# Kernel optimization log

Hardware: AMD Instinct MI355X
Metric: run time of the kernel (lower is better)

Reference implementation:

```python
import jax, jax.numpy as jnp
import numpy as np

B, L, D = 16384, 32, 128
DIAG_LEN, PROC_LEN, MED_LEN = 100000, 50000, 1000


def setup_inputs() -> dict:
    key = jax.random.key(0)
    ks = jax.random.split(key, 12)
    inp = {
        "diag_codes": jax.random.randint(ks[0], (B, L), 0, DIAG_LEN),
        "proc_codes": jax.random.randint(ks[1], (B, L), 0, PROC_LEN),
        "prev_diag_codes": jax.random.randint(ks[2], (B, L), 0, DIAG_LEN),
        "prev_proc_codes": jax.random.randint(ks[3], (B, L), 0, PROC_LEN),
        # learned parameters (torch Linear convention: W[out,in], y = x @ W.T + b)
        "diag_emb": jax.random.normal(ks[4], (DIAG_LEN, D), jnp.float32) * 0.02,
        "proc_emb": jax.random.normal(ks[5], (PROC_LEN, D), jnp.float32) * 0.02,
        "W1": jax.random.normal(ks[6], (D, 2 * D), jnp.float32) * 0.02,
        "b1": jnp.zeros((D,), jnp.float32),
        "W2": jax.random.normal(ks[7], (256, 2 * D), jnp.float32) * 0.02,
        "b2": jnp.zeros((256,), jnp.float32),
        "W3": jax.random.normal(ks[8], (MED_LEN, 256), jnp.float32) * 0.02,
        "b3": jnp.zeros((MED_LEN,), jnp.float32),
    }
    return inp


def _bag_sum(table, idx):
    # EmbeddingBag('sum'): gather [B,L,D] then reduce over codes -> [B,D]
    return jnp.take(table, idx, axis=0).sum(axis=1)


def reference(diag_codes, proc_codes, prev_diag_codes, prev_proc_codes,
              diag_emb, proc_emb, W1, b1, W2, b2, W3, b3):
    emb_d = _bag_sum(diag_emb, diag_codes)            # [B,128]
    emb_p = _bag_sum(proc_emb, proc_codes)            # [B,128]
    prev_d = _bag_sum(diag_emb, prev_diag_codes)      # [B,128]
    prev_p = _bag_sum(proc_emb, prev_proc_codes)      # [B,128]

    # health_net = Linear(256->128) + Dropout (identity in eval mode)
    cur = jnp.concatenate([emb_d, emb_p], axis=1) @ W1.T + b1     # [B,128]
    prev = jnp.concatenate([prev_d, prev_p], axis=1) @ W1.T + b1  # [B,128]

    rep = jnp.concatenate([cur, prev], axis=1)        # [B,256]
    h = jax.nn.relu(rep @ W2.T + b2)                  # [B,256]
    return jax.nn.sigmoid(h @ W3.T + b3)              # [B,med_len]
```

## Files before the change

kernel.cpp:

```cpp
#include <hip/hip_runtime.h>
#include <hip/hip_bf16.h>
#include <math.h>

#define NB 16384
#define MED 1000
#define MD 100000
#define MP 50000
#define TDB 512
#define TPB 256
#define CD 3125
#define CP 1563
#define NCV 1280
#define FP8_SCALE 4096.0f
#define FP8_INV   (1.0f / 4096.0f)

typedef __bf16 bf16x8 __attribute__((ext_vector_type(8)));
typedef float  f32x4  __attribute__((ext_vector_type(4)));
typedef float  f32x2  __attribute__((ext_vector_type(2)));
typedef unsigned short u16;
typedef unsigned int   u32;
typedef unsigned char  u8;

__device__ __forceinline__ u16 f2bf(float f) {
    union { float f; u32 u; } v; v.f = f;
    u32 r = v.u + 0x7fffu + ((v.u >> 16) & 1u);
    return (u16)(r >> 16);
}
__device__ __forceinline__ u32 fbits(float f) { union { float f; u32 u; } v; v.f = f; return v.u; }

__device__ __forceinline__ u32 pktr(float lo, float hi) {
    return (fbits(lo) >> 16) | (fbits(hi) & 0xffff0000u);
}
__device__ __forceinline__ bf16x8 pk8(const float4 a, const float4 b) {
    union { u32 u[4]; bf16x8 v; } r;
    r.u[0] = pktr(a.x, a.y); r.u[1] = pktr(a.z, a.w);
    r.u[2] = pktr(b.x, b.y); r.u[3] = pktr(b.z, b.w);
    return r.v;
}

__global__ __launch_bounds__(256, 2) void prep_kernel(
    const float* __restrict__ Ed, const float* __restrict__ Ep,
    const float* __restrict__ W1,
    const float* __restrict__ W2, const float* __restrict__ W3,
    u8* __restrict__ Td, u8* __restrict__ Tp,
    u16* __restrict__ W2b, u16* __restrict__ W3b)
{
    const int bid = blockIdx.x, tid = threadIdx.x;

    if (bid >= TDB + TPB) {
        int i = (bid - (TDB + TPB)) * 256 + tid;
        if (i < 65536) { W2b[i] = f2bf(W2[i]); return; }
        i -= 65536;
        if (i < 262144) W3b[i] = (i < MED * 256) ? f2bf(W3[i]) : (u16)0;
        return;
    }

    const float* E; u8* T; int M, koff, c0, nblk, nch;
    if (bid < TDB) { E = Ed; T = Td; M = MD; koff = 0;   c0 = bid;       nblk = TDB; nch = CD; }
    else           { E = Ep; T = Tp; M = MP; koff = 128; c0 = bid - TDB; nblk = TPB; nch = CP; }

    const int wave = tid >> 6, lane = tid & 63;
    const int quad = lane >> 4, l16 = lane & 15;
    const int colBase = (wave & 1) * 64;
    const int rowOff  = (wave >> 1) * 16;

    bf16x8 a[4][4];
    #pragma unroll
    for (int mt = 0; mt < 4; ++mt) {
        const float* wp = W1 + (size_t)(colBase + mt * 16 + l16) * 256 + koff + quad * 8;
        #pragma unroll
        for (int ks = 0; ks < 4; ++ks) {
            const float4 lo = *(const float4*)(wp + ks * 32);
            const float4 hi = *(const float4*)(wp + ks * 32 + 4);
            union { u16 s[8]; bf16x8 v; } r;
            r.s[0]=f2bf(lo.x); r.s[1]=f2bf(lo.y); r.s[2]=f2bf(lo.z); r.s[3]=f2bf(lo.w);
            r.s[4]=f2bf(hi.x); r.s[5]=f2bf(hi.y); r.s[6]=f2bf(hi.z); r.s[7]=f2bf(hi.w);
            a[mt][ks] = r.v;
        }
    }

    float4 cur[8];
    {
        const int row = min(c0 * 32 + rowOff + l16, M - 1);
        const float* p = E + (size_t)row * 128 + quad * 8;
        #pragma unroll
        for (int ks = 0; ks < 4; ++ks) {
            cur[ks * 2]     = *(const float4*)(p + ks * 32);
            cur[ks * 2 + 1] = *(const float4*)(p + ks * 32 + 4);
        }
    }

    #pragma unroll 1
    for (int c = c0; c < nch; c += nblk) {
        float4 nxt[8];
        const int cn = c + nblk;
        if (cn < nch) {
            const int row = min(cn * 32 + rowOff + l16, M - 1);
            const float* p = E + (size_t)row * 128 + quad * 8;
            #pragma unroll
            for (int ks = 0; ks < 4; ++ks) {
                nxt[ks * 2]     = *(const float4*)(p + ks * 32);
                nxt[ks * 2 + 1] = *(const float4*)(p + ks * 32 + 4);
            }
        }

        bf16x8 b[4];
        #pragma unroll
        for (int ks = 0; ks < 4; ++ks) b[ks] = pk8(cur[ks * 2], cur[ks * 2 + 1]);

        f32x4 acc[4];
        #pragma unroll
        for (int mt = 0; mt < 4; ++mt) acc[mt] = (f32x4){0.f, 0.f, 0.f, 0.f};
        #pragma unroll
        for (int ks = 0; ks < 4; ++ks)
            #pragma unroll
            for (int mt = 0; mt < 4; ++mt)
                acc[mt] = __builtin_amdgcn_mfma_f32_16x16x32_bf16(a[mt][ks], b[ks], acc[mt], 0, 0, 0);

        const int row = c * 32 + rowOff + l16;
        if (row < M) {
            u8* rp = T + (size_t)row * 128 + colBase + quad * 4;
            #pragma unroll
            for (int mt = 0; mt < 4; ++mt) {
                const f32x4 v = acc[mt];
                int p = __builtin_amdgcn_cvt_pk_fp8_f32(v[0] * FP8_SCALE, v[1] * FP8_SCALE, 0, 0);
                p = __builtin_amdgcn_cvt_pk_fp8_f32(v[2] * FP8_SCALE, v[3] * FP8_SCALE, p, 1);
                *(u32*)(rp + mt * 16) = (u32)p;
            }
        }

        #pragma unroll
        for (int j = 0; j < 8; ++j) cur[j] = nxt[j];
    }
}

__global__ __launch_bounds__(256) void gather_rep(
    const int* __restrict__ diag, const int* __restrict__ proc,
    const int* __restrict__ pdiag, const int* __restrict__ pproc,
    const u8* __restrict__ Td, const u8* __restrict__ Tp,
    const float* __restrict__ b1, u16* __restrict__ rep)
{
    __shared__ int   sidx[8 * 4 * 33];
    __shared__ float sred[8][2][8][16];
    const int t = threadIdx.x;

    for (int i = t; i < 1024; i += 256) {
        const int s = i >> 7, bg = (i >> 5) & 3, l = i & 31;
        const int* cp = (bg == 0) ? diag : (bg == 1) ? proc : (bg == 2) ? pdiag : pproc;
        sidx[(s * 4 + bg) * 33 + l] = cp[(blockIdx.x * 8 + s) * 32 + l];
    }
    __syncthreads();

    const int sub = t >> 5, bag = (t >> 3) & 3, lc = t & 7;
    const u8* tbl = (bag & 1) ? Tp : Td;
    const int* myidx = &sidx[(sub * 4 + bag) * 33];

    f32x2 s[8];
    #pragma unroll
    for (int i = 0; i < 8; ++i) s[i] = (f32x2){0.f, 0.f};

    uint4 va[8], vb[8];
    #pragma unroll
    for (int j = 0; j < 8; ++j)
        va[j] = *(const uint4*)(tbl + (size_t)myidx[j] * 128 + lc * 16);
    #pragma unroll
    for (int j = 0; j < 8; ++j)
        vb[j] = *(const uint4*)(tbl + (size_t)myidx[8 + j] * 128 + lc * 16);

#define CONSUME(V) do { \
    _Pragma("unroll") \
    for (int j = 0; j < 8; ++j) { \
        s[0] += __builtin_amdgcn_cvt_pk_f32_fp8((int)V[j].x, 0); \
        s[1] += __builtin_amdgcn_cvt_pk_f32_fp8((int)V[j].x, 1); \
        s[2] += __builtin_amdgcn_cvt_pk_f32_fp8((int)V[j].y, 0); \
        s[3] += __builtin_amdgcn_cvt_pk_f32_fp8((int)V[j].y, 1); \
        s[4] += __builtin_amdgcn_cvt_pk_f32_fp8((int)V[j].z, 0); \
        s[5] += __builtin_amdgcn_cvt_pk_f32_fp8((int)V[j].z, 1); \
        s[6] += __builtin_amdgcn_cvt_pk_f32_fp8((int)V[j].w, 0); \
        s[7] += __builtin_amdgcn_cvt_pk_f32_fp8((int)V[j].w, 1); \
    } } while (0)

    {
        uint4 tmp[8];
        #pragma unroll
        for (int j = 0; j < 8; ++j)
            tmp[j] = *(const uint4*)(tbl + (size_t)myidx[16 + j] * 128 + lc * 16);
        CONSUME(va);
        #pragma unroll
        for (int j = 0; j < 8; ++j) va[j] = tmp[j];
    }
    {
        uint4 tmp[8];
        #pragma unroll
        for (int j = 0; j < 8; ++j)
            tmp[j] = *(const uint4*)(tbl + (size_t)myidx[24 + j] * 128 + lc * 16);
        CONSUME(vb);
        #pragma unroll
        for (int j = 0; j < 8; ++j) vb[j] = tmp[j];
    }
    CONSUME(va);
    CONSUME(vb);
#undef CONSUME

    const int half = bag >> 1;
    if (bag & 1) {
        float* dst = &sred[sub][half][lc][0];
        #pragma unroll
        for (int i = 0; i < 4; ++i)
            *(f32x4*)(dst + i * 4) = (f32x4){s[2*i].x, s[2*i].y, s[2*i+1].x, s[2*i+1].y};
    }
    __syncthreads();
    if (!(bag & 1)) {
        const float* par = &sred[sub][half][lc][0];
        const float* bp  = b1 + lc * 16;
        u32 o[8];
        #pragma unroll
        for (int i = 0; i < 8; ++i) {
            const float e0 = (s[i].x + par[2*i])   * FP8_INV + bp[2*i];
            const float e1 = (s[i].y + par[2*i+1]) * FP8_INV + bp[2*i+1];
            o[i] = (u32)f2bf(e0) | ((u32)f2bf(e1) << 16);
        }
        const int b = blockIdx.x * 8 + sub;
        u16* dst = rep + (size_t)b * 256 + half * 128 + lc * 16;
        *(uint4*)dst       = make_uint4(o[0], o[1], o[2], o[3]);
        *(uint4*)(dst + 8) = make_uint4(o[4], o[5], o[6], o[7]);
    }
}

__global__ __launch_bounds__(256, 2) void gemm2(
    const u16* __restrict__ rep, const u16* __restrict__ W2b,
    const float* __restrict__ b2, u16* __restrict__ h)
{
    const int wave = threadIdx.x >> 6, lane = threadIdx.x & 63;
    const int quad = lane >> 4, l16 = lane & 15;
    const int nBase = blockIdx.x * 64;
    const int mChunk = blockIdx.y * 128;

    bf16x8 w[4][8];
    #pragma unroll
    for (int nt = 0; nt < 4; ++nt) {
        const u16* wP = W2b + (size_t)(nBase + nt * 16 + l16) * 256 + quad * 8;
        #pragma unroll
        for (int ks = 0; ks < 8; ++ks) w[nt][ks] = *(const bf16x8*)(wP + ks * 32);
    }
    float bv[4];
    #pragma unroll
    for (int nt = 0; nt < 4; ++nt) bv[nt] = b2[nBase + nt * 16 + l16];

    const u16* aP = rep + (size_t)(mChunk + wave * 16 + l16) * 256 + quad * 8;
    bf16x8 a[8];
    #pragma unroll
    for (int ks = 0; ks < 8; ++ks) a[ks] = *(const bf16x8*)(aP + ks * 32);

    #pragma unroll 1
    for (int iter = 0; iter < 2; ++iter) {
        bf16x8 an[8];
        if (iter < 1) {
            const u16* aN = aP + 64 * 256;
            #pragma unroll
            for (int ks = 0; ks < 8; ++ks) an[ks] = *(const bf16x8*)(aN + ks * 32);
        }
        f32x4 acc[4];
        #pragma unroll
        for (int nt = 0; nt < 4; ++nt) acc[nt] = (f32x4){0.f,0.f,0.f,0.f};
        #pragma unroll
        for (int ks = 0; ks < 8; ++ks)
            #pragma unroll
            for (int nt = 0; nt < 4; ++nt)
                acc[nt] = __builtin_amdgcn_mfma_f32_16x16x32_bf16(a[ks], w[nt][ks], acc[nt], 0, 0, 0);

        const int rowB = mChunk + iter * 64 + wave * 16 + quad * 4;
        #pragma unroll
        for (int nt = 0; nt < 4; ++nt) {
            const int col = nBase + nt * 16 + l16;
            #pragma unroll
            for (int r = 0; r < 4; ++r) {
                float v = acc[nt][r] + bv[nt];
                v = v > 0.f ? v : 0.f;
                h[(size_t)(rowB + r) * 256 + col] = f2bf(v);
            }
        }
        if (iter < 1) {
            aP += 64 * 256;
            #pragma unroll
            for (int ks = 0; ks < 8; ++ks) a[ks] = an[ks];
        }
    }
}

__global__ __launch_bounds__(256, 2) void gemm3(
    const u16* __restrict__ h, const u16* __restrict__ W3b,
    const float* __restrict__ b3, float* __restrict__ out)
{
    const int wave = threadIdx.x >> 6, lane = threadIdx.x & 63;
    const int quad = lane >> 4, l16 = lane & 15;
    const int nBase = blockIdx.x * 64;
    const int mChunk = blockIdx.y * 512;

    bf16x8 w[4][8];
    #pragma unroll
    for (int nt = 0; nt < 4; ++nt) {
        const u16* wP = W3b + (size_t)(nBase + nt * 16 + l16) * 256 + quad * 8;
        #pragma unroll
        for (int ks = 0; ks < 8; ++ks) w[nt][ks] = *(const bf16x8*)(wP + ks * 32);
    }
    float bv[4]; int colv[4];
    #pragma unroll
    for (int nt = 0; nt < 4; ++nt) {
        colv[nt] = nBase + nt * 16 + l16;
        bv[nt] = (colv[nt] < MED) ? b3[colv[nt]] : 0.f;
    }

    const u16* aP = h + (size_t)(mChunk + wave * 16 + l16) * 256 + quad * 8;
    bf16x8 a[8];
    #pragma unroll
    for (int ks = 0; ks < 8; ++ks) a[ks] = *(const bf16x8*)(aP + ks * 32);

    #pragma unroll 1
    for (int iter = 0; iter < 8; ++iter) {
        bf16x8 an[8];
        if (iter < 7) {
            const u16* aN = aP + 64 * 256;
            #pragma unroll
            for (int ks = 0; ks < 8; ++ks) an[ks] = *(const bf16x8*)(aN + ks * 32);
        }
        f32x4 acc[4];
        #pragma unroll
        for (int nt = 0; nt < 4; ++nt) acc[nt] = (f32x4){0.f,0.f,0.f,0.f};
        #pragma unroll
        for (int ks = 0; ks < 8; ++ks)
            #pragma unroll
            for (int nt = 0; nt < 4; ++nt)
                acc[nt] = __builtin_amdgcn_mfma_f32_16x16x32_bf16(a[ks], w[nt][ks], acc[nt], 0, 0, 0);

        const int rowB = mChunk + iter * 64 + wave * 16 + quad * 4;
        #pragma unroll
        for (int nt = 0; nt < 4; ++nt) {
            if (colv[nt] < MED) {
                #pragma unroll
                for (int r = 0; r < 4; ++r) {
                    const float v = acc[nt][r] + bv[nt];
                    const float e = __expf(-v);
                    out[(size_t)(rowB + r) * MED + colv[nt]] = __builtin_amdgcn_rcpf(1.0f + e);
                }
            }
        }
        if (iter < 7) {
            aP += 64 * 256;
            #pragma unroll
            for (int ks = 0; ks < 8; ++ks) a[ks] = an[ks];
        }
    }
}

extern "C" void kernel_launch(void* const* d_in, const int* in_sizes, int n_in,
                              void* d_out, int out_size, void* d_ws, size_t ws_size,
                              hipStream_t stream)
{
    const int*   diag  = (const int*)d_in[0];
    const int*   proc  = (const int*)d_in[1];
    const int*   pdiag = (const int*)d_in[2];
    const int*   pproc = (const int*)d_in[3];
    const float* demb  = (const float*)d_in[4];
    const float* pemb  = (const float*)d_in[5];
    const float* W1    = (const float*)d_in[6];
    const float* b1    = (const float*)d_in[7];
    const float* W2    = (const float*)d_in[8];
    const float* b2    = (const float*)d_in[9];
    const float* W3    = (const float*)d_in[10];
    const float* b3    = (const float*)d_in[11];

    char* ws = (char*)d_ws;
    u8*  Td  = (u8*)ws;
    u8*  Tp  = (u8*)(ws + 12800000);
    u16* rep = (u16*)(ws + 19200000);
    u16* W2b = (u16*)(ws + 27588608);
    u16* W3b = (u16*)(ws + 27719680);
    u16* h   = (u16*)ws;

    prep_kernel<<<TDB + TPB + NCV, 256, 0, stream>>>(demb, pemb, W1, W2, W3, Td, Tp, W2b, W3b);
    gather_rep<<<NB / 8, 256, 0, stream>>>(diag, proc, pdiag, pproc, Td, Tp, b1, rep);
    gemm2<<<dim3(4, 128), 256, 0, stream>>>(rep, W2b, b2, h);
    gemm3<<<dim3(16, 32), 256, 0, stream>>>(h, W3b, b3, (float*)d_out);
}
```

Measured before the change: 245.9 us.

## Replace persistent prefetch loop in prep_kernel with one 64-row tile per block

The embedding-table transform (E @ W1 slice, quantized to fp8) previously used a fixed grid of persistent blocks that looped over 32-row chunks with software prefetch. Each block now handles exactly one 64-row tile, with each wave computing two 16-row n-tiles, and the grid grows to cover the whole table. All embedding loads are issued up front before the W1 fragment conversion, and the per-block loop and prefetch bookkeeping are removed. In exchange, every block reloads and converts W1 to bf16, adding redundant weight traffic across many more blocks.

```diff
diff --git a/kernel.cpp b/kernel.cpp
--- a/kernel.cpp
+++ b/kernel.cpp
@@ -6,10 +6,9 @@
 #define MED 1000
 #define MD 100000
 #define MP 50000
-#define TDB 512
-#define TPB 256
-#define CD 3125
-#define CP 1563
+#define TDB64 1563
+#define TPB64 782
+#define NTR2 (TDB64 + TPB64)
 #define NCV 1280
 #define FP8_SCALE 4096.0f
 #define FP8_INV   (1.0f / 4096.0f)
@@ -47,22 +46,34 @@
 {
     const int bid = blockIdx.x, tid = threadIdx.x;
 
-    if (bid >= TDB + TPB) {
-        int i = (bid - (TDB + TPB)) * 256 + tid;
+    if (bid >= NTR2) {
+        int i = (bid - NTR2) * 256 + tid;
         if (i < 65536) { W2b[i] = f2bf(W2[i]); return; }
         i -= 65536;
         if (i < 262144) W3b[i] = (i < MED * 256) ? f2bf(W3[i]) : (u16)0;
         return;
     }
 
-    const float* E; u8* T; int M, koff, c0, nblk, nch;
-    if (bid < TDB) { E = Ed; T = Td; M = MD; koff = 0;   c0 = bid;       nblk = TDB; nch = CD; }
-    else           { E = Ep; T = Tp; M = MP; koff = 128; c0 = bid - TDB; nblk = TPB; nch = CP; }
+    const float* E; u8* T; int M, koff, blk;
+    if (bid < TDB64) { E = Ed; T = Td; M = MD; koff = 0;   blk = bid; }
+    else             { E = Ep; T = Tp; M = MP; koff = 128; blk = bid - TDB64; }
 
     const int wave = tid >> 6, lane = tid & 63;
     const int quad = lane >> 4, l16 = lane & 15;
     const int colBase = (wave & 1) * 64;
-    const int rowOff  = (wave >> 1) * 16;
+    const int rowBase = blk * 64 + (wave >> 1) * 32;
+
+    float4 e[2][8];
+    #pragma unroll
+    for (int nt = 0; nt < 2; ++nt) {
+        const int row = min(rowBase + nt * 16 + l16, M - 1);
+        const float* p = E + (size_t)row * 128 + quad * 8;
+        #pragma unroll
+        for (int ks = 0; ks < 4; ++ks) {
+            e[nt][ks * 2]     = *(const float4*)(p + ks * 32);
+            e[nt][ks * 2 + 1] = *(const float4*)(p + ks * 32 + 4);
+        }
+    }
 
     bf16x8 a[4][4];
     #pragma unroll
@@ -79,58 +90,37 @@
         }
     }
 
-    float4 cur[8];
-    {
-        const int row = min(c0 * 32 + rowOff + l16, M - 1);
-        const float* p = E + (size_t)row * 128 + quad * 8;
-        #pragma unroll
-        for (int ks = 0; ks < 4; ++ks) {
-            cur[ks * 2]     = *(const float4*)(p + ks * 32);
-            cur[ks * 2 + 1] = *(const float4*)(p + ks * 32 + 4);
-        }
-    }
-
-    #pragma unroll 1
-    for (int c = c0; c < nch; c += nblk) {
-        float4 nxt[8];
-        const int cn = c + nblk;
-        if (cn < nch) {
-            const int row = min(cn * 32 + rowOff + l16, M - 1);
-            const float* p = E + (size_t)row * 128 + quad * 8;
-            #pragma unroll
-            for (int ks = 0; ks < 4; ++ks) {
-                nxt[ks * 2]     = *(const float4*)(p + ks * 32);
-                nxt[ks * 2 + 1] = *(const float4*)(p + ks * 32 + 4);
-            }
-        }
-
-        bf16x8 b[4];
-        #pragma unroll
-        for (int ks = 0; ks < 4; ++ks) b[ks] = pk8(cur[ks * 2], cur[ks * 2 + 1]);
-
-        f32x4 acc[4];
-        #pragma unroll
-        for (int mt = 0; mt < 4; ++mt) acc[mt] = (f32x4){0.f, 0.f, 0.f, 0.f};
-        #pragma unroll
-        for (int ks = 0; ks < 4; ++ks)
-            #pragma unroll
-            for (int mt = 0; mt < 4; ++mt)
-                acc[mt] = __builtin_amdgcn_mfma_f32_16x16x32_bf16(a[mt][ks], b[ks], acc[mt], 0, 0, 0);
-
-        const int row = c * 32 + rowOff + l16;
-        if (row < M) {
-            u8* rp = T + (size_t)row * 128 + colBase + quad * 4;
+    f32x4 acc[4][2];
+    #pragma unroll
+    for (int mt = 0; mt < 4; ++mt) {
+        acc[mt][0] = (f32x4){0.f,0.f,0.f,0.f};
+        acc[mt][1] = (f32x4){0.f,0.f,0.f,0.f};
+    }
+
+    #pragma unroll
+    for (int ks = 0; ks < 4; ++ks) {
+        const bf16x8 b0 = pk8(e[0][ks * 2], e[0][ks * 2 + 1]);
+        const bf16x8 b1 = pk8(e[1][ks * 2], e[1][ks * 2 + 1]);
+        #pragma unroll
+        for (int mt = 0; mt < 4; ++mt) {
+            acc[mt][0] = __builtin_amdgcn_mfma_f32_16x16x32_bf16(a[mt][ks], b0, acc[mt][0], 0, 0, 0);
+            acc[mt][1] = __builtin_amdgcn_mfma_f32_16x16x32_bf16(a[mt][ks], b1, acc[mt][1], 0, 0, 0);
+        }
+    }
+
+    #pragma unroll
+    for (int nt = 0; nt < 2; ++nt) {
+        const int rn = rowBase + nt * 16 + l16;
+        if (rn < M) {
+            u8* rp = T + (size_t)rn * 128 + colBase + quad * 4;
             #pragma unroll
             for (int mt = 0; mt < 4; ++mt) {
-                const f32x4 v = acc[mt];
+                const f32x4 v = acc[mt][nt];
                 int p = __builtin_amdgcn_cvt_pk_fp8_f32(v[0] * FP8_SCALE, v[1] * FP8_SCALE, 0, 0);
                 p = __builtin_amdgcn_cvt_pk_fp8_f32(v[2] * FP8_SCALE, v[3] * FP8_SCALE, p, 1);
                 *(u32*)(rp + mt * 16) = (u32)p;
             }
         }
-
-        #pragma unroll
-        for (int j = 0; j < 8; ++j) cur[j] = nxt[j];
     }
 }
 
@@ -378,7 +368,7 @@
     u16* W3b = (u16*)(ws + 27719680);
     u16* h   = (u16*)ws;
 
-    prep_kernel<<<TDB + TPB + NCV, 256, 0, stream>>>(demb, pemb, W1, W2, W3, Td, Tp, W2b, W3b);
+    prep_kernel<<<NTR2 + NCV, 256, 0, stream>>>(demb, pemb, W1, W2, W3, Td, Tp, W2b, W3b);
     gather_rep<<<NB / 8, 256, 0, stream>>>(diag, proc, pdiag, pproc, Td, Tp, b1, rep);
     gemm2<<<dim3(4, 128), 256, 0, stream>>>(rep, W2b, b2, h);
     gemm3<<<dim3(16, 32), 256, 0, stream>>>(h, W3b, b3, (float*)d_out);
```

Result: slower. 268.9 us (+9.3%).
